# Kernel tuning notes

Measured on AMD Instinct MI355X. Metric: run time of the kernel, lower is better.

## Reference

```python
import jax, jax.numpy as jnp
import numpy as np

B, T, D = 512, 128, 256
L, CH, CS = 3, 128, 10
H = L * CH            # hidden_dim = 384
G = 4 * H + 2 * L     # gate projection width = 1542
HS = H // 6           # 64


def setup_inputs() -> dict:
    key = jax.random.key(0)
    ks = jax.random.split(key, 12)
    def lin(k, out_d, in_d):
        return jax.random.normal(k, (out_d, in_d), jnp.float32) * (1.0 / np.sqrt(in_d))
    return {
        "x": jax.random.normal(ks[0], (B, T, D), jnp.float32),
        "time": jax.random.uniform(ks[1], (B, T), jnp.float32),
        "kW": lin(ks[2], G, D + 1), "kb": jnp.zeros((G,), jnp.float32),
        "rW": lin(ks[3], G, H + 1), "rb": jnp.zeros((G,), jnp.float32),
        "sW": lin(ks[4], HS, H), "sb": jnp.zeros((HS,), jnp.float32),
        "rsW": lin(ks[5], H, HS), "rsb": jnp.zeros((H,), jnp.float32),
        "cW": lin(ks[6], H, H * CS).reshape(H, H, CS), "cb": jnp.zeros((H,), jnp.float32),
    }


def _cumax_l2r(z):
    return jnp.cumsum(jax.nn.softmax(z, axis=-1), axis=-1)


def _cumax_r2l(z):
    zf = jnp.flip(z, -1)
    return jnp.flip(jnp.cumsum(jax.nn.softmax(zf, axis=-1), axis=-1), -1)


def _forward(x, time, kW, kb, rW, rb, sW, sb, rsW, rsb, cW, cb):
    def step(carry, xt):
        c, h, buf_h, buf_d = carry
        xi, ti = xt                      # xi: (B,D), ti: (B,)
        ti = ti[:, None]
        xo = (jnp.concatenate([xi, ti], -1) @ kW.T + kb
              + jnp.concatenate([h, ti], -1) @ rW.T + rb)   # (B,G)
        fm = _cumax_l2r(xo[:, :L])[:, :, None]              # (B,L,1) master forget
        im = _cumax_r2l(xo[:, L:2 * L])[:, :, None]         # (B,L,1) master input
        g = xo[:, 2 * L:].reshape(-1, 4 * L, CH)
        fg = jax.nn.sigmoid(g[:, :L])
        ig = jax.nn.sigmoid(g[:, L:2 * L])
        og = jax.nn.sigmoid(g[:, 2 * L:3 * L])
        ci = jnp.tanh(g[:, 3 * L:])
        cl = c.reshape(-1, L, CH)
        ov = fm * im
        cn = ov * (fg * cl + ig * ci) + (fm - ov) * cl + (im - ov) * ci
        hn = og * jnp.tanh(cn)
        c_flat = cn.reshape(-1, H)
        h_flat = hn.reshape(-1, H)
        cur_dis = 1.0 - jnp.mean(fm[..., 0], axis=-1)       # (B,)
        buf_h = jnp.concatenate([buf_h[1:], h_flat[None]], 0)   # (CS,B,H)
        buf_d = jnp.concatenate([buf_d[1:], cur_dis[None]], 0)  # (CS,B)
        local_dis = jax.nn.softmax(jnp.cumsum(buf_d.T, axis=1), axis=1)  # (B,CS)
        local_h = buf_h.transpose(1, 2, 0) * local_dis[:, None, :]       # (B,H,CS)
        theme = jnp.mean(local_h, axis=-1)                               # (B,H)
        theme = jax.nn.sigmoid(jax.nn.relu(theme @ sW.T + sb) @ rsW.T + rsb)
        conv = jnp.einsum('bck,ock->bo', local_h, cW) + cb   # Conv1d over full window
        local = theme * conv
        return (c_flat, h_flat, buf_h, buf_d), (h_flat, local, cur_dis)

    z = jnp.zeros((x.shape[0], H), jnp.float32)
    carry0 = (z, z,
              jnp.zeros((CS, x.shape[0], H), jnp.float32),
              jnp.zeros((CS, x.shape[0]), jnp.float32))
    _, (origin_h, hs, dist) = jax.lax.scan(
        step, carry0, (x.transpose(1, 0, 2), time.T))
    output = hs.transpose(1, 0, 2) + origin_h.transpose(1, 0, 2)  # (B,T,H)
    last_output = output[:, -1, :]
    return last_output, output, dist  # dist: (T,B)


def reference(x, time, kW, kb, rW, rb, sW, sb, rsW, rsb, cW, cb):
    return _forward(x, time, kW, kb, rW, rb, sW, sb, rsW, rsb, cW, cb)
```

## Files before the change

kernel.cpp:

```cpp
#include <hip/hip_runtime.h>
#include <math.h>

typedef unsigned short u16;
typedef __attribute__((ext_vector_type(8))) short bf16x8;
typedef __attribute__((ext_vector_type(4))) float f32x4;

#define MFMA(a, b, c) __builtin_amdgcn_mfma_f32_16x16x32_bf16(a, b, c, 0, 0, 0)

#define Bsz 512
#define Tsz 128
#define Dsz 256
#define CSs 10
#define Hsz 384
#define Gsz 1542
#define HSz 64
#define Gp  1568
#define NGT 98
#define KTH 12
#define KTX 8
#define KTC 120

constexpr size_t O_WPK  = 0;
constexpr size_t O_XWPK = O_WPK  + 2ull*NGT*KTH*2*512;
constexpr size_t O_CPK  = O_XWPK + 2ull*NGT*KTX*2*512;
constexpr size_t O_SPK  = O_CPK  + 2ull*24*KTC*512;
constexpr size_t O_RPK  = O_SPK  + 2ull*4*KTH*2*512;
constexpr size_t O_BC   = O_RPK  + 2ull*24*2*2*512;
constexpr size_t O_WT   = O_BC + 4ull*Gp;
constexpr size_t O_HBF  = (O_WT + 4ull*Gp + 255) & ~(size_t)255;
constexpr size_t O_XPK  = O_HBF + 2ull*Bsz*Tsz*Hsz;
constexpr size_t O_XWB  = O_XPK + 2ull*Tsz*32*KTX*2*512;
constexpr size_t O_HWB  = O_XWB + 4ull*2*Bsz*Gp;
constexpr size_t O_CFB  = O_HWB + 4ull*2*Bsz*Gp;
constexpr size_t ZERO_BEG = O_CFB;
constexpr size_t ZERO_END = O_CFB + 4ull*2*Bsz*Hsz;

__device__ __forceinline__ u16 f2bf(float f) {
    unsigned u = __float_as_uint(f);
    unsigned r = (u + 0x7FFFu + ((u >> 16) & 1u)) >> 16;
    return (u16)r;
}
__device__ __forceinline__ float bf2f(u16 v) {
    return __uint_as_float(((unsigned)v) << 16);
}
__device__ __forceinline__ float sigm(float v) { return 1.f / (1.f + expf(-v)); }

__global__ __launch_bounds__(256) void zero4(float4* __restrict__ p, int n4) {
    int i = blockIdx.x * 256 + threadIdx.x;
    if (i < n4) p[i] = make_float4(0.f, 0.f, 0.f, 0.f);
}

__global__ __launch_bounds__(256) void build_w(const float* __restrict__ kW,
                                               const float* __restrict__ kb,
                                               const float* __restrict__ rW,
                                               const float* __restrict__ rb,
                                               const float* __restrict__ sW,
                                               const float* __restrict__ rsW,
                                               u16* __restrict__ wpk,
                                               u16* __restrict__ xwpk,
                                               u16* __restrict__ spk,
                                               u16* __restrict__ rpk,
                                               float* __restrict__ bc,
                                               float* __restrict__ wt) {
    const int N1 = Gp * 384, N2 = Gp * 256, N3 = 64 * 384, N4 = 384 * 64;
    int idx = blockIdx.x * 256 + threadIdx.x;
    if (idx < N1) {
        int g = idx / 384, k = idx % 384;
        float v = (g < Gsz) ? rW[g * (Hsz + 1) + k] : 0.f;
        u16 hi = f2bf(v), lo = f2bf(v - bf2f(hi));
        size_t fo = ((size_t)((g >> 4) * KTH + (k >> 5)) * 2) * 512;
        int pos = ((g & 15) | (((k >> 3) & 3) << 4)) * 8 + (k & 7);
        wpk[fo + pos] = hi; wpk[fo + 512 + pos] = lo;
    } else if (idx < N1 + N2) {
        int i = idx - N1;
        int g = i / 256, k = i % 256;
        float v = (g < Gsz) ? kW[g * (Dsz + 1) + k] : 0.f;
        u16 hi = f2bf(v), lo = f2bf(v - bf2f(hi));
        size_t fo = ((size_t)((g >> 4) * KTX + (k >> 5)) * 2) * 512;
        int pos = ((g & 15) | (((k >> 3) & 3) << 4)) * 8 + (k & 7);
        xwpk[fo + pos] = hi; xwpk[fo + 512 + pos] = lo;
    } else if (idx < N1 + N2 + N3) {
        int i = idx - N1 - N2;
        int g = i / 384, k = i % 384;
        float v = sW[g * Hsz + k];
        u16 hi = f2bf(v), lo = f2bf(v - bf2f(hi));
        size_t fo = ((size_t)((g >> 4) * KTH + (k >> 5)) * 2) * 512;
        int pos = ((g & 15) | (((k >> 3) & 3) << 4)) * 8 + (k & 7);
        spk[fo + pos] = hi; spk[fo + 512 + pos] = lo;
    } else if (idx < N1 + N2 + N3 + N4) {
        int i = idx - N1 - N2 - N3;
        int g = i / 64, k = i % 64;
        float v = rsW[g * HSz + k];
        u16 hi = f2bf(v), lo = f2bf(v - bf2f(hi));
        size_t fo = ((size_t)((g >> 4) * 2 + (k >> 5)) * 2) * 512;
        int pos = ((g & 15) | (((k >> 3) & 3) << 4)) * 8 + (k & 7);
        rpk[fo + pos] = hi; rpk[fo + 512 + pos] = lo;
    } else if (idx < N1 + N2 + N3 + N4 + Gsz) {
        int g = idx - N1 - N2 - N3 - N4;
        bc[g] = kb[g] + rb[g];
        wt[g] = kW[g * (Dsz + 1) + Dsz] + rW[g * (Hsz + 1) + Hsz];
    }
}

__global__ __launch_bounds__(256) void pack_x(const float* __restrict__ x,
                                              u16* __restrict__ xpk) {
    int idx = blockIdx.x * 256 + threadIdx.x;
    int k = idx & 255, b = (idx >> 8) & 511, t = idx >> 17;
    float v = x[((size_t)b * Tsz + t) * Dsz + k];
    u16 hi = f2bf(v), lo = f2bf(v - bf2f(hi));
    size_t fo = (((size_t)t * 32 + (b >> 4)) * KTX + (k >> 5)) * 2 * 512;
    int pos = ((b & 15) | (((k >> 3) & 3) << 4)) * 8 + (k & 7);
    xpk[fo + pos] = hi;
    xpk[fo + 512 + pos] = lo;
}

__global__ __launch_bounds__(256) void pack_cw(const float* __restrict__ cW,
                                               u16* __restrict__ cpk) {
    int idx = blockIdx.x * 256 + threadIdx.x;
    if (idx >= Hsz * Hsz * CSs) return;
    int o = idx / (Hsz * CSs), kk = idx % (Hsz * CSs);
    int ch = kk / CSs, jj = kk % CSs;
    int k2 = jj * Hsz + ch;
    size_t fo = ((size_t)(o >> 4) * KTC + (k2 >> 5)) * 512;
    int pos = ((o & 15) | (((k2 >> 3) & 3) << 4)) * 8 + (k2 & 7);
    cpk[fo + pos] = f2bf(cW[idx]);
}

__global__ __launch_bounds__(448) void fused(const float* __restrict__ tme,
                                             char* __restrict__ ws,
                                             float* __restrict__ out, int t) {
    const u16* wpk  = (const u16*)(ws + O_WPK);
    const u16* xwpk = (const u16*)(ws + O_XWPK);
    const u16* xpk  = (const u16*)(ws + O_XPK);
    const float* bc = (const float*)(ws + O_BC);
    const float* wt = (const float*)(ws + O_WT);
    float* xw = (float*)(ws + O_XWB);
    float* hw = (float*)(ws + O_HWB);
    float* cf = (float*)(ws + O_CFB);
    u16* hbf = (u16*)(ws + O_HBF);
    float* out_seq  = out + (size_t)Bsz * Hsz;
    float* out_dist = out_seq + (size_t)Bsz * Tsz * Hsz;

    int bid = blockIdx.x;
    int tid = threadIdx.x;
    int wave = tid >> 6, lane = tid & 63, l15 = lane & 15, lk = lane >> 4;
    int role = bid >> 8;
    int q = bid & 255;
    int mt = q >> 3, sbp = q & 7;

    __shared__ u16 s_h[KTH][2][512];
    __shared__ float s_fi[16][4];

    if (role == 1) {
        if (t >= Tsz) return;
        int base = sbp * 12 + (sbp < 2 ? sbp : 2);
        int cnt  = (sbp < 2) ? 13 : 12;
        const u16* Asrc = xpk + ((size_t)(t * 32 + mt) * KTX * 2) * 512;
        bf16x8 ah[KTX], al[KTX];
        #pragma unroll
        for (int kt = 0; kt < KTX; ++kt) {
            ah[kt] = *(const bf16x8*)(Asrc + (size_t)(kt * 2) * 512 + lane * 8);
            al[kt] = *(const bf16x8*)(Asrc + (size_t)(kt * 2 + 1) * 512 + lane * 8);
        }
        float* dst = xw + (size_t)(t & 1) * Bsz * Gp;
        #pragma unroll
        for (int ti = 0; ti < 2; ++ti) {
            int idx = 2 * wave + ti;
            if (idx < cnt) {
                int gt = base + idx;
                f32x4 acc = {};
                #pragma unroll
                for (int half = 0; half < 2; ++half) {
                    bf16x8 bh[4], bl[4];
                    #pragma unroll
                    for (int kk = 0; kk < 4; ++kk) {
                        int kt = half * 4 + kk;
                        size_t fb = ((size_t)(gt * KTX + kt) * 2) * 512 + lane * 8;
                        bh[kk] = *(const bf16x8*)(xwpk + fb);
                        bl[kk] = *(const bf16x8*)(xwpk + fb + 512);
                    }
                    #pragma unroll
                    for (int kk = 0; kk < 4; ++kk) {
                        int kt = half * 4 + kk;
                        acc = MFMA(ah[kt], bh[kk], acc);
                        acc = MFMA(ah[kt], bl[kk], acc);
                        acc = MFMA(al[kt], bh[kk], acc);
                    }
                }
                int col = gt * 16 + l15;
                #pragma unroll
                for (int j = 0; j < 4; ++j)
                    dst[(size_t)(mt * 16 + lk * 4 + j) * Gp + col] = acc[j];
            }
        }
        return;
    }
    if (sbp == 7) return;

    if (t == 0) {
        for (int i = tid; i < KTH * 2 * 256; i += 448) ((unsigned*)s_h)[i] = 0u;
    } else {
        const float* xw1 = xw + (size_t)((t - 1) & 1) * Bsz * Gp;
        const float* hw1 = hw + (size_t)((t - 1) & 1) * Bsz * Gp;
        const float* cfo = cf + (size_t)(t & 1) * Bsz * Hsz;
        float* cfn = cf + (size_t)((t - 1) & 1) * Bsz * Hsz;
        if (tid < 16) {
            int r = tid, b = mt * 16 + r;
            float tv = tme[b * Tsz + (t - 1)];
            const float* xr = xw1 + (size_t)b * Gp;
            const float* hr = hw1 + (size_t)b * Gp;
            float zf[6];
            #pragma unroll
            for (int g = 0; g < 6; ++g)
                zf[g] = xr[g] + hr[g] + bc[g] + tv * wt[g];
            float m = fmaxf(zf[0], fmaxf(zf[1], zf[2]));
            float e0 = expf(zf[0] - m), e1 = expf(zf[1] - m), e2 = expf(zf[2] - m);
            float inv = 1.f / (e0 + e1 + e2);
            float fm0 = e0 * inv, fm1 = fm0 + e1 * inv;
            float mw = fmaxf(zf[3], fmaxf(zf[4], zf[5]));
            float f0 = expf(zf[3] - mw), f1 = expf(zf[4] - mw), f2 = expf(zf[5] - mw);
            float invw = 1.f / (f0 + f1 + f2);
            float im2 = f2 * invw, im1 = f1 * invw + im2;
            s_fi[r][0] = fm0; s_fi[r][1] = fm1; s_fi[r][2] = im1; s_fi[r][3] = im2;
            if (sbp == 0)
                out_dist[(size_t)(t - 1) * Bsz + b] = 1.f - (fm0 + fm1 + 1.f) * (1.f / 3.f);
        }
        __syncthreads();
        if (tid < Hsz) {
            int ch = tid;
            int l = ch >> 7;
            int kt = ch >> 5;
            int g0 = 6 + ch, g1 = g0 + Hsz, g2 = g0 + 2 * Hsz, g3 = g0 + 3 * Hsz;
            float bcg0 = bc[g0], bcg1 = bc[g1], bcg2 = bc[g2], bcg3 = bc[g3];
            float wtg0 = wt[g0], wtg1 = wt[g1], wtg2 = wt[g2], wtg3 = wt[g3];
            const float* xr = xw1 + (size_t)(mt * 16) * Gp;
            const float* hr = hw1 + (size_t)(mt * 16) * Gp;
            float nx0 = xr[g0], nx1 = xr[g1], nx2 = xr[g2], nx3 = xr[g3];
            float nh0 = hr[g0], nh1 = hr[g1], nh2 = hr[g2], nh3 = hr[g3];
            for (int r = 0; r < 16; ++r) {
                float cx0 = nx0, cx1 = nx1, cx2 = nx2, cx3 = nx3;
                float hv0 = nh0, hv1 = nh1, hv2 = nh2, hv3 = nh3;
                if (r < 15) {
                    const float* xr2 = xr + (size_t)(r + 1) * Gp;
                    const float* hr2 = hr + (size_t)(r + 1) * Gp;
                    nx0 = xr2[g0]; nx1 = xr2[g1]; nx2 = xr2[g2]; nx3 = xr2[g3];
                    nh0 = hr2[g0]; nh1 = hr2[g1]; nh2 = hr2[g2]; nh3 = hr2[g3];
                }
                int b = mt * 16 + r;
                float tv = tme[b * Tsz + (t - 1)];
                float fm = (l == 0) ? s_fi[r][0] : ((l == 1) ? s_fi[r][1] : 1.f);
                float im = (l == 0) ? 1.f : ((l == 1) ? s_fi[r][2] : s_fi[r][3]);
                float fg = sigm(cx0 + hv0 + bcg0 + tv * wtg0);
                float ig = sigm(cx1 + hv1 + bcg1 + tv * wtg1);
                float og = sigm(cx2 + hv2 + bcg2 + tv * wtg2);
                float ci = tanhf(cx3 + hv3 + bcg3 + tv * wtg3);
                float cl = cfo[(size_t)b * Hsz + ch];
                float ov = fm * im;
                float cn = ov * (fg * cl + ig * ci) + (fm - ov) * cl + (im - ov) * ci;
                float hn = og * tanhf(cn);
                u16 hh = f2bf(hn);
                u16 hl = f2bf(hn - bf2f(hh));
                if (sbp == 0) {
                    cfn[(size_t)b * Hsz + ch] = cn;
                    size_t oi = ((size_t)b * Tsz + (t - 1)) * Hsz + ch;
                    out_seq[oi] = hn;
                    hbf[oi] = hh;
                }
                int pos = (r | (((ch >> 3) & 3) << 4)) * 8 + (ch & 7);
                s_h[kt][0][pos] = hh;
                s_h[kt][1][pos] = hl;
            }
        }
    }
    __syncthreads();
    if (t >= Tsz) return;

    float* dst = hw + (size_t)(t & 1) * Bsz * Gp;
    #pragma unroll
    for (int ti = 0; ti < 2; ++ti) {
        int gt = sbp * 14 + wave * 2 + ti;
        f32x4 acc = {};
        #pragma unroll
        for (int half = 0; half < 2; ++half) {
            bf16x8 bh[6], bl[6];
            #pragma unroll
            for (int kk = 0; kk < 6; ++kk) {
                int kt = half * 6 + kk;
                size_t fb = ((size_t)(gt * KTH + kt) * 2) * 512 + lane * 8;
                bh[kk] = *(const bf16x8*)(wpk + fb);
                bl[kk] = *(const bf16x8*)(wpk + fb + 512);
            }
            #pragma unroll
            for (int kk = 0; kk < 6; ++kk) {
                int kt = half * 6 + kk;
                bf16x8 ah = *(const bf16x8*)&s_h[kt][0][lane * 8];
                bf16x8 al = *(const bf16x8*)&s_h[kt][1][lane * 8];
                acc = MFMA(ah, bh[kk], acc);
                acc = MFMA(ah, bl[kk], acc);
                acc = MFMA(al, bh[kk], acc);
            }
        }
        int col = gt * 16 + l15;
        #pragma unroll
        for (int j = 0; j < 4; ++j)
            dst[(size_t)(mt * 16 + lk * 4 + j) * Gp + col] = acc[j];
    }
}

__global__ __launch_bounds__(512, 1) void post(const float* __restrict__ sb,
                                               const float* __restrict__ rsb,
                                               const float* __restrict__ cb,
                                               char* __restrict__ ws,
                                               float* __restrict__ out) {
    const u16* cpk = (const u16*)(ws + O_CPK);
    const u16* spk = (const u16*)(ws + O_SPK);
    const u16* rpk = (const u16*)(ws + O_RPK);
    const u16* hbf = (const u16*)(ws + O_HBF);

    float* out_last = out;
    float* out_seq  = out + (size_t)Bsz * Hsz;
    const float* out_dist = out_seq + (size_t)Bsz * Tsz * Hsz;

    int b = blockIdx.x, t0 = blockIdx.y * 16;
    int tid = threadIdx.x;
    int wave = tid >> 6, lane = tid & 63, l15 = lane & 15, lk = lane >> 4;

    __shared__ u16 s_apk[KTC][512];
    __shared__ u16 s_tpk[KTH * 2][512];
    __shared__ float th1s[16][68];
    __shared__ float s_ld[16][CSs];

    if (tid < 16) {
        int r = tid;
        float vals[CSs];
        float cum = 0.f;
        #pragma unroll
        for (int j = 0; j < CSs; ++j) {
            int tp = t0 + r - 9 + j;
            float d = (tp < 0) ? 0.f : out_dist[(size_t)tp * Bsz + b];
            cum += d;
            vals[j] = cum;
        }
        float mx = vals[0];
        #pragma unroll
        for (int j = 1; j < CSs; ++j) mx = fmaxf(mx, vals[j]);
        float sum = 0.f;
        #pragma unroll
        for (int j = 0; j < CSs; ++j) { vals[j] = expf(vals[j] - mx); sum += vals[j]; }
        float invs = 1.f / sum;
        #pragma unroll
        for (int j = 0; j < CSs; ++j) s_ld[r][j] = vals[j] * invs;
    }
    __syncthreads();

    for (int u = tid; u < 768; u += 512) {
        int c8 = u >> 4, r = u & 15;
        int ch0 = c8 * 8;
        int rowoff = c8 >> 2;
        int pos16 = (r | ((c8 & 3) << 4)) * 8;
        bf16x8 hv[CSs];
        #pragma unroll
        for (int j = 0; j < CSs; ++j) {
            int tp = t0 + r - 9 + j;
            bf16x8 z = {};
            hv[j] = (tp >= 0) ? *(const bf16x8*)(hbf + ((size_t)b * Tsz + tp) * Hsz + ch0) : z;
        }
        float acc[8] = {0.f, 0.f, 0.f, 0.f, 0.f, 0.f, 0.f, 0.f};
        #pragma unroll
        for (int j = 0; j < CSs; ++j) {
            float ldv = s_ld[r][j];
            bf16x8 av8;
            #pragma unroll
            for (int e = 0; e < 8; ++e) {
                float av = bf2f((u16)hv[j][e]) * ldv;
                acc[e] += av;
                av8[e] = (short)f2bf(av);
            }
            *(bf16x8*)&s_apk[j * 12 + rowoff][pos16] = av8;
        }
        bf16x8 th8, tl8;
        #pragma unroll
        for (int e = 0; e < 8; ++e) {
            float thm = acc[e] * 0.1f;
            u16 th = f2bf(thm);
            th8[e] = (short)th;
            tl8[e] = (short)f2bf(thm - bf2f(th));
        }
        int kt2 = rowoff * 2;
        *(bf16x8*)&s_tpk[kt2][pos16] = th8;
        *(bf16x8*)&s_tpk[kt2 + 1][pos16] = tl8;
    }
    __syncthreads();

    f32x4 cacc[3] = {};
    for (int k0 = 0; k0 < KTC; k0 += 8) {
        bf16x8 bv[3][8];
        #pragma unroll
        for (int kk = 0; kk < 8; ++kk)
            #pragma unroll
            for (int i = 0; i < 3; ++i)
                bv[i][kk] = *(const bf16x8*)(cpk + ((size_t)((wave * 3 + i) * KTC + k0 + kk)) * 512 + lane * 8);
        #pragma unroll
        for (int kk = 0; kk < 8; ++kk) {
            bf16x8 a = *(const bf16x8*)&s_apk[k0 + kk][lane * 8];
            #pragma unroll
            for (int i = 0; i < 3; ++i)
                cacc[i] = MFMA(a, bv[i][kk], cacc[i]);
        }
    }
    if (wave < 4) {
        f32x4 a1 = {};
        for (int kt = 0; kt < KTH; ++kt) {
            bf16x8 ah = *(const bf16x8*)&s_tpk[kt * 2][lane * 8];
            bf16x8 al = *(const bf16x8*)&s_tpk[kt * 2 + 1][lane * 8];
            size_t bb = ((size_t)(wave * KTH + kt) * 2) * 512 + lane * 8;
            bf16x8 bh = *(const bf16x8*)(spk + bb);
            bf16x8 bl = *(const bf16x8*)(spk + bb + 512);
            a1 = MFMA(ah, bh, a1);
            a1 = MFMA(ah, bl, a1);
            a1 = MFMA(al, bh, a1);
        }
        int col = wave * 16 + l15;
        #pragma unroll
        for (int j = 0; j < 4; ++j)
            th1s[lk * 4 + j][col] = fmaxf(a1[j] + sb[col], 0.f);
    }
    __syncthreads();

    bf16x8 ah2[2], al2[2];
    #pragma unroll
    for (int kt = 0; kt < 2; ++kt) {
        bf16x8 zh, zl;
        #pragma unroll
        for (int e = 0; e < 8; ++e) {
            float v = th1s[l15][kt * 32 + lk * 8 + e];
            u16 hi = f2bf(v);
            zh[e] = (short)hi;
            zl[e] = (short)f2bf(v - bf2f(hi));
        }
        ah2[kt] = zh; al2[kt] = zl;
    }
    #pragma unroll
    for (int i = 0; i < 3; ++i) {
        int ot = wave * 3 + i;
        f32x4 a2 = {};
        #pragma unroll
        for (int kt = 0; kt < 2; ++kt) {
            size_t bb = ((size_t)(ot * 2 + kt) * 2) * 512 + lane * 8;
            bf16x8 bh = *(const bf16x8*)(rpk + bb);
            bf16x8 bl = *(const bf16x8*)(rpk + bb + 512);
            a2 = MFMA(ah2[kt], bh, a2);
            a2 = MFMA(ah2[kt], bl, a2);
            a2 = MFMA(al2[kt], bh, a2);
        }
        int col = ot * 16 + l15;
        #pragma unroll
        for (int j = 0; j < 4; ++j) {
            int row = lk * 4 + j;
            int tt = t0 + row;
            size_t oi = ((size_t)b * Tsz + tt) * Hsz + col;
            float convv = cacc[i][j] + cb[col];
            float th = sigm(a2[j] + rsb[col]);
            float val = th * convv + out_seq[oi];
            out_seq[oi] = val;
            if (tt == Tsz - 1) out_last[(size_t)b * Hsz + col] = val;
        }
    }
}

extern "C" void kernel_launch(void* const* d_in, const int* in_sizes, int n_in,
                              void* d_out, int out_size, void* d_ws, size_t ws_size,
                              hipStream_t stream) {
    const float* x   = (const float*)d_in[0];
    const float* tme = (const float*)d_in[1];
    const float* kW  = (const float*)d_in[2];
    const float* kb  = (const float*)d_in[3];
    const float* rW  = (const float*)d_in[4];
    const float* rb  = (const float*)d_in[5];
    const float* sW  = (const float*)d_in[6];
    const float* sb  = (const float*)d_in[7];
    const float* rsW = (const float*)d_in[8];
    const float* rsb = (const float*)d_in[9];
    const float* cW  = (const float*)d_in[10];
    const float* cb  = (const float*)d_in[11];

    char* wsb = (char*)d_ws;
    float* outp = (float*)d_out;

    u16* wpk  = (u16*)(wsb + O_WPK);
    u16* xwpk = (u16*)(wsb + O_XWPK);
    u16* cpk  = (u16*)(wsb + O_CPK);
    u16* spk  = (u16*)(wsb + O_SPK);
    u16* rpk  = (u16*)(wsb + O_RPK);
    float* bc = (float*)(wsb + O_BC);
    float* wt = (float*)(wsb + O_WT);
    u16* xpk  = (u16*)(wsb + O_XPK);

    zero4<<<(int)((ZERO_END - ZERO_BEG) / 16 + 255) / 256, 256, 0, stream>>>(
        (float4*)(wsb + ZERO_BEG), (int)((ZERO_END - ZERO_BEG) / 16));
    {
        int nW = Gp * 384 + Gp * 256 + 64 * 384 + 384 * 64 + Gsz;
        build_w<<<(nW + 255) / 256, 256, 0, stream>>>(kW, kb, rW, rb, sW, rsW,
                                                      wpk, xwpk, spk, rpk, bc, wt);
    }
    pack_x<<<(Tsz * Bsz * Dsz) / 256, 256, 0, stream>>>(x, xpk);
    pack_cw<<<(Hsz * Hsz * CSs + 255) / 256, 256, 0, stream>>>(cW, cpk);

    for (int t = 0; t <= Tsz; ++t)
        fused<<<512, 448, 0, stream>>>(tme, wsb, outp, t);
    post<<<dim3(Bsz, Tsz / 16), 512, 0, stream>>>(sb, rsb, cb, wsb, outp);
}
```

Before: 3.682 ms.

## Precompute input projection for all timesteps in one batched kernel before recurrence

The x@kW input projection for every timestep is computed up front in a single large kernel into a workspace buffer, instead of being computed by half of the blocks inside each per-step fused launch. The recurrent launches then use half the grid and read the precomputed slice for step t-1. This moves off-critical-path work out of the sequential loop, at the cost of about 400MB of extra workspace and extra memory traffic. It falls back to the old path if the workspace is too small.

```diff
diff --git a/kernel.cpp b/kernel.cpp
--- a/kernel.cpp
+++ b/kernel.cpp
@@ -15,6 +15,7 @@
 #define Gsz 1542
 #define HSz 64
 #define Gp  1568
+#define BG  ((size_t)Bsz * Gp)
 #define NGT 98
 #define KTH 12
 #define KTX 8
@@ -30,10 +31,12 @@
 constexpr size_t O_HBF  = (O_WT + 4ull*Gp + 255) & ~(size_t)255;
 constexpr size_t O_XPK  = O_HBF + 2ull*Bsz*Tsz*Hsz;
 constexpr size_t O_XWB  = O_XPK + 2ull*Tsz*32*KTX*2*512;
-constexpr size_t O_HWB  = O_XWB + 4ull*2*Bsz*Gp;
-constexpr size_t O_CFB  = O_HWB + 4ull*2*Bsz*Gp;
+constexpr size_t O_HWB  = O_XWB + 4ull*2*BG;
+constexpr size_t O_CFB  = O_HWB + 4ull*2*BG;
 constexpr size_t ZERO_BEG = O_CFB;
 constexpr size_t ZERO_END = O_CFB + 4ull*2*Bsz*Hsz;
+constexpr size_t O_XWALL = (ZERO_END + 255) & ~(size_t)255;
+constexpr size_t NEED_ALL = O_XWALL + 4ull*Tsz*BG;
 
 __device__ __forceinline__ u16 f2bf(float f) {
     unsigned u = __float_as_uint(f);
@@ -126,9 +129,67 @@
     cpk[fo + pos] = f2bf(cW[idx]);
 }
 
+__device__ __forceinline__ void xw_slab(const u16* __restrict__ xwpk,
+                                        const u16* __restrict__ xpk,
+                                        float* __restrict__ dst,
+                                        int t, int mt, int sbp,
+                                        int wave, int lane, int l15, int lk) {
+    int base = sbp * 12 + (sbp < 2 ? sbp : 2);
+    int cnt  = (sbp < 2) ? 13 : 12;
+    const u16* Asrc = xpk + ((size_t)(t * 32 + mt) * KTX * 2) * 512;
+    bf16x8 ah[KTX], al[KTX];
+    #pragma unroll
+    for (int kt = 0; kt < KTX; ++kt) {
+        ah[kt] = *(const bf16x8*)(Asrc + (size_t)(kt * 2) * 512 + lane * 8);
+        al[kt] = *(const bf16x8*)(Asrc + (size_t)(kt * 2 + 1) * 512 + lane * 8);
+    }
+    #pragma unroll
+    for (int ti = 0; ti < 2; ++ti) {
+        int idx = 2 * wave + ti;
+        if (idx < cnt) {
+            int gt = base + idx;
+            f32x4 acc = {};
+            #pragma unroll
+            for (int half = 0; half < 2; ++half) {
+                bf16x8 bh[4], bl[4];
+                #pragma unroll
+                for (int kk = 0; kk < 4; ++kk) {
+                    int kt = half * 4 + kk;
+                    size_t fb = ((size_t)(gt * KTX + kt) * 2) * 512 + lane * 8;
+                    bh[kk] = *(const bf16x8*)(xwpk + fb);
+                    bl[kk] = *(const bf16x8*)(xwpk + fb + 512);
+                }
+                #pragma unroll
+                for (int kk = 0; kk < 4; ++kk) {
+                    int kt = half * 4 + kk;
+                    acc = MFMA(ah[kt], bh[kk], acc);
+                    acc = MFMA(ah[kt], bl[kk], acc);
+                    acc = MFMA(al[kt], bh[kk], acc);
+                }
+            }
+            int col = gt * 16 + l15;
+            #pragma unroll
+            for (int j = 0; j < 4; ++j)
+                dst[(size_t)(mt * 16 + lk * 4 + j) * Gp + col] = acc[j];
+        }
+    }
+}
+
+__global__ __launch_bounds__(448) void xwall_k(char* __restrict__ ws) {
+    const u16* xwpk = (const u16*)(ws + O_XWPK);
+    const u16* xpk  = (const u16*)(ws + O_XPK);
+    float* xwall = (float*)(ws + O_XWALL);
+    int q = blockIdx.x, t = blockIdx.y;
+    int mt = q >> 3, sbp = q & 7;
+    int wave = threadIdx.x >> 6, lane = threadIdx.x & 63;
+    xw_slab(xwpk, xpk, xwall + (size_t)t * BG, t, mt, sbp,
+            wave, lane, lane & 15, lane >> 4);
+}
+
 __global__ __launch_bounds__(448) void fused(const float* __restrict__ tme,
                                              char* __restrict__ ws,
-                                             float* __restrict__ out, int t) {
+                                             float* __restrict__ out, int t,
+                                             int use_all) {
     const u16* wpk  = (const u16*)(ws + O_WPK);
     const u16* xwpk = (const u16*)(ws + O_XWPK);
     const u16* xpk  = (const u16*)(ws + O_XPK);
@@ -153,46 +214,8 @@
 
     if (role == 1) {
         if (t >= Tsz) return;
-        int base = sbp * 12 + (sbp < 2 ? sbp : 2);
-        int cnt  = (sbp < 2) ? 13 : 12;
-        const u16* Asrc = xpk + ((size_t)(t * 32 + mt) * KTX * 2) * 512;
-        bf16x8 ah[KTX], al[KTX];
-        #pragma unroll
-        for (int kt = 0; kt < KTX; ++kt) {
-            ah[kt] = *(const bf16x8*)(Asrc + (size_t)(kt * 2) * 512 + lane * 8);
-            al[kt] = *(const bf16x8*)(Asrc + (size_t)(kt * 2 + 1) * 512 + lane * 8);
-        }
-        float* dst = xw + (size_t)(t & 1) * Bsz * Gp;
-        #pragma unroll
-        for (int ti = 0; ti < 2; ++ti) {
-            int idx = 2 * wave + ti;
-            if (idx < cnt) {
-                int gt = base + idx;
-                f32x4 acc = {};
-                #pragma unroll
-                for (int half = 0; half < 2; ++half) {
-                    bf16x8 bh[4], bl[4];
-                    #pragma unroll
-                    for (int kk = 0; kk < 4; ++kk) {
-                        int kt = half * 4 + kk;
-                        size_t fb = ((size_t)(gt * KTX + kt) * 2) * 512 + lane * 8;
-                        bh[kk] = *(const bf16x8*)(xwpk + fb);
-                        bl[kk] = *(const bf16x8*)(xwpk + fb + 512);
-                    }
-                    #pragma unroll
-                    for (int kk = 0; kk < 4; ++kk) {
-                        int kt = half * 4 + kk;
-                        acc = MFMA(ah[kt], bh[kk], acc);
-                        acc = MFMA(ah[kt], bl[kk], acc);
-                        acc = MFMA(al[kt], bh[kk], acc);
-                    }
-                }
-                int col = gt * 16 + l15;
-                #pragma unroll
-                for (int j = 0; j < 4; ++j)
-                    dst[(size_t)(mt * 16 + lk * 4 + j) * Gp + col] = acc[j];
-            }
-        }
+        float* dst = xw + (size_t)(t & 1) * BG;
+        xw_slab(xwpk, xpk, dst, t, mt, sbp, wave, lane, l15, lk);
         return;
     }
     if (sbp == 7) return;
@@ -200,8 +223,9 @@
     if (t == 0) {
         for (int i = tid; i < KTH * 2 * 256; i += 448) ((unsigned*)s_h)[i] = 0u;
     } else {
-        const float* xw1 = xw + (size_t)((t - 1) & 1) * Bsz * Gp;
-        const float* hw1 = hw + (size_t)((t - 1) & 1) * Bsz * Gp;
+        const float* xw1 = use_all ? (const float*)(ws + O_XWALL) + (size_t)(t - 1) * BG
+                                   : xw + (size_t)((t - 1) & 1) * BG;
+        const float* hw1 = hw + (size_t)((t - 1) & 1) * BG;
         const float* cfo = cf + (size_t)(t & 1) * Bsz * Hsz;
         float* cfn = cf + (size_t)((t - 1) & 1) * Bsz * Hsz;
         if (tid < 16) {
@@ -275,7 +299,7 @@
     __syncthreads();
     if (t >= Tsz) return;
 
-    float* dst = hw + (size_t)(t & 1) * Bsz * Gp;
+    float* dst = hw + (size_t)(t & 1) * BG;
     #pragma unroll
     for (int ti = 0; ti < 2; ++ti) {
         int gt = sbp * 14 + wave * 2 + ti;
@@ -496,6 +520,8 @@
     float* wt = (float*)(wsb + O_WT);
     u16* xpk  = (u16*)(wsb + O_XPK);
 
+    int use_all = (ws_size >= NEED_ALL) ? 1 : 0;
+
     zero4<<<(int)((ZERO_END - ZERO_BEG) / 16 + 255) / 256, 256, 0, stream>>>(
         (float4*)(wsb + ZERO_BEG), (int)((ZERO_END - ZERO_BEG) / 16));
     {
@@ -506,7 +532,11 @@
     pack_x<<<(Tsz * Bsz * Dsz) / 256, 256, 0, stream>>>(x, xpk);
     pack_cw<<<(Hsz * Hsz * CSs + 255) / 256, 256, 0, stream>>>(cW, cpk);
 
+    if (use_all)
+        xwall_k<<<dim3(256, Tsz), 448, 0, stream>>>(wsb);
+
+    int grid = use_all ? 256 : 512;
     for (int t = 0; t <= Tsz; ++t)
-        fused<<<512, 448, 0, stream>>>(tme, wsb, outp, t);
+        fused<<<grid, 448, 0, stream>>>(tme, wsb, outp, t, use_all);
     post<<<dim3(Bsz, Tsz / 16), 512, 0, stream>>>(sb, rsb, cb, wsb, outp);
 }
```

Result: no change. 3.660 ms (-0.6%).

## Merge x-projection and recurrent roles into one 1024-thread block per tile

Applied to the files above, without the earlier changes.

The per-step kernel used to launch 512 blocks of 448 threads, half computing the input projection and half the recurrent update plus hidden projection. It now launches 256 blocks of 1024 threads, each doing both jobs. Each wave handles one gate tile instead of two, and the elementwise cell update is split across twice as many threads, eight rows each instead of sixteen. The aim is to shorten the serial per-step critical path through more wave-level parallelism, at the cost of bigger blocks with one block per CU and more register pressure.

```diff
diff --git a/kernel.cpp b/kernel.cpp
--- a/kernel.cpp
+++ b/kernel.cpp
@@ -15,6 +15,7 @@
 #define Gsz 1542
 #define HSz 64
 #define Gp  1568
+#define BG  ((size_t)Bsz * Gp)
 #define NGT 98
 #define KTH 12
 #define KTX 8
@@ -30,8 +31,8 @@
 constexpr size_t O_HBF  = (O_WT + 4ull*Gp + 255) & ~(size_t)255;
 constexpr size_t O_XPK  = O_HBF + 2ull*Bsz*Tsz*Hsz;
 constexpr size_t O_XWB  = O_XPK + 2ull*Tsz*32*KTX*2*512;
-constexpr size_t O_HWB  = O_XWB + 4ull*2*Bsz*Gp;
-constexpr size_t O_CFB  = O_HWB + 4ull*2*Bsz*Gp;
+constexpr size_t O_HWB  = O_XWB + 4ull*2*BG;
+constexpr size_t O_CFB  = O_HWB + 4ull*2*BG;
 constexpr size_t ZERO_BEG = O_CFB;
 constexpr size_t ZERO_END = O_CFB + 4ull*2*Bsz*Hsz;
 
@@ -126,9 +127,9 @@
     cpk[fo + pos] = f2bf(cW[idx]);
 }
 
-__global__ __launch_bounds__(448) void fused(const float* __restrict__ tme,
-                                             char* __restrict__ ws,
-                                             float* __restrict__ out, int t) {
+__global__ __launch_bounds__(1024, 1) void fused(const float* __restrict__ tme,
+                                                 char* __restrict__ ws,
+                                                 float* __restrict__ out, int t) {
     const u16* wpk  = (const u16*)(ws + O_WPK);
     const u16* xwpk = (const u16*)(ws + O_XWPK);
     const u16* xpk  = (const u16*)(ws + O_XPK);
@@ -144,166 +145,159 @@
     int bid = blockIdx.x;
     int tid = threadIdx.x;
     int wave = tid >> 6, lane = tid & 63, l15 = lane & 15, lk = lane >> 4;
-    int role = bid >> 8;
-    int q = bid & 255;
-    int mt = q >> 3, sbp = q & 7;
+    int mt = bid >> 3, sbp = bid & 7;
 
     __shared__ u16 s_h[KTH][2][512];
     __shared__ float s_fi[16][4];
 
-    if (role == 1) {
-        if (t >= Tsz) return;
+    if (sbp < 7) {
+        if (t == 0) {
+            for (int i = tid; i < KTH * 2 * 256; i += 1024) ((unsigned*)s_h)[i] = 0u;
+        } else {
+            const float* xw1 = xw + (size_t)((t - 1) & 1) * BG;
+            const float* hw1 = hw + (size_t)((t - 1) & 1) * BG;
+            const float* cfo = cf + (size_t)(t & 1) * Bsz * Hsz;
+            float* cfn = cf + (size_t)((t - 1) & 1) * Bsz * Hsz;
+            if (tid < 16) {
+                int r = tid, b = mt * 16 + r;
+                float tv = tme[b * Tsz + (t - 1)];
+                const float* xr = xw1 + (size_t)b * Gp;
+                const float* hr = hw1 + (size_t)b * Gp;
+                float zf[6];
+                #pragma unroll
+                for (int g = 0; g < 6; ++g)
+                    zf[g] = xr[g] + hr[g] + bc[g] + tv * wt[g];
+                float m = fmaxf(zf[0], fmaxf(zf[1], zf[2]));
+                float e0 = expf(zf[0] - m), e1 = expf(zf[1] - m), e2 = expf(zf[2] - m);
+                float inv = 1.f / (e0 + e1 + e2);
+                float fm0 = e0 * inv, fm1 = fm0 + e1 * inv;
+                float mw = fmaxf(zf[3], fmaxf(zf[4], zf[5]));
+                float f0 = expf(zf[3] - mw), f1 = expf(zf[4] - mw), f2 = expf(zf[5] - mw);
+                float invw = 1.f / (f0 + f1 + f2);
+                float im2 = f2 * invw, im1 = f1 * invw + im2;
+                s_fi[r][0] = fm0; s_fi[r][1] = fm1; s_fi[r][2] = im1; s_fi[r][3] = im2;
+                if (sbp == 0)
+                    out_dist[(size_t)(t - 1) * Bsz + b] = 1.f - (fm0 + fm1 + 1.f) * (1.f / 3.f);
+            }
+            __syncthreads();
+            if (tid < 768) {
+                int ch = tid >> 1;
+                int rh = tid & 1;
+                int l = ch >> 7;
+                int kt = ch >> 5;
+                int g0 = 6 + ch, g1 = g0 + Hsz, g2 = g0 + 2 * Hsz, g3 = g0 + 3 * Hsz;
+                float bcg0 = bc[g0], bcg1 = bc[g1], bcg2 = bc[g2], bcg3 = bc[g3];
+                float wtg0 = wt[g0], wtg1 = wt[g1], wtg2 = wt[g2], wtg3 = wt[g3];
+                const float* xr = xw1 + (size_t)(mt * 16 + rh * 8) * Gp;
+                const float* hr = hw1 + (size_t)(mt * 16 + rh * 8) * Gp;
+                float nx0 = xr[g0], nx1 = xr[g1], nx2 = xr[g2], nx3 = xr[g3];
+                float nh0 = hr[g0], nh1 = hr[g1], nh2 = hr[g2], nh3 = hr[g3];
+                for (int r2 = 0; r2 < 8; ++r2) {
+                    float cx0 = nx0, cx1 = nx1, cx2 = nx2, cx3 = nx3;
+                    float hv0 = nh0, hv1 = nh1, hv2 = nh2, hv3 = nh3;
+                    if (r2 < 7) {
+                        const float* xr2 = xr + (size_t)(r2 + 1) * Gp;
+                        const float* hr2 = hr + (size_t)(r2 + 1) * Gp;
+                        nx0 = xr2[g0]; nx1 = xr2[g1]; nx2 = xr2[g2]; nx3 = xr2[g3];
+                        nh0 = hr2[g0]; nh1 = hr2[g1]; nh2 = hr2[g2]; nh3 = hr2[g3];
+                    }
+                    int r = rh * 8 + r2;
+                    int b = mt * 16 + r;
+                    float tv = tme[b * Tsz + (t - 1)];
+                    float fm = (l == 0) ? s_fi[r][0] : ((l == 1) ? s_fi[r][1] : 1.f);
+                    float im = (l == 0) ? 1.f : ((l == 1) ? s_fi[r][2] : s_fi[r][3]);
+                    float fg = sigm(cx0 + hv0 + bcg0 + tv * wtg0);
+                    float ig = sigm(cx1 + hv1 + bcg1 + tv * wtg1);
+                    float og = sigm(cx2 + hv2 + bcg2 + tv * wtg2);
+                    float ci = tanhf(cx3 + hv3 + bcg3 + tv * wtg3);
+                    float cl = cfo[(size_t)b * Hsz + ch];
+                    float ov = fm * im;
+                    float cn = ov * (fg * cl + ig * ci) + (fm - ov) * cl + (im - ov) * ci;
+                    float hn = og * tanhf(cn);
+                    u16 hh = f2bf(hn);
+                    u16 hl = f2bf(hn - bf2f(hh));
+                    if (sbp == 0) {
+                        cfn[(size_t)b * Hsz + ch] = cn;
+                        size_t oi = ((size_t)b * Tsz + (t - 1)) * Hsz + ch;
+                        out_seq[oi] = hn;
+                        hbf[oi] = hh;
+                    }
+                    int pos = (r | (((ch >> 3) & 3) << 4)) * 8 + (ch & 7);
+                    s_h[kt][0][pos] = hh;
+                    s_h[kt][1][pos] = hl;
+                }
+            }
+        }
+        __syncthreads();
+
+        if (t < Tsz && wave < 14) {
+            int gt = sbp * 14 + wave;
+            float* dst = hw + (size_t)(t & 1) * BG;
+            f32x4 acc = {};
+            #pragma unroll
+            for (int half = 0; half < 2; ++half) {
+                bf16x8 bh[6], bl[6];
+                #pragma unroll
+                for (int kk = 0; kk < 6; ++kk) {
+                    int kt = half * 6 + kk;
+                    size_t fb = ((size_t)(gt * KTH + kt) * 2) * 512 + lane * 8;
+                    bh[kk] = *(const bf16x8*)(wpk + fb);
+                    bl[kk] = *(const bf16x8*)(wpk + fb + 512);
+                }
+                #pragma unroll
+                for (int kk = 0; kk < 6; ++kk) {
+                    int kt = half * 6 + kk;
+                    bf16x8 ah = *(const bf16x8*)&s_h[kt][0][lane * 8];
+                    bf16x8 al = *(const bf16x8*)&s_h[kt][1][lane * 8];
+                    acc = MFMA(ah, bh[kk], acc);
+                    acc = MFMA(ah, bl[kk], acc);
+                    acc = MFMA(al, bh[kk], acc);
+                }
+            }
+            int col = gt * 16 + l15;
+            #pragma unroll
+            for (int j = 0; j < 4; ++j)
+                dst[(size_t)(mt * 16 + lk * 4 + j) * Gp + col] = acc[j];
+        }
+    }
+
+    if (t < Tsz) {
         int base = sbp * 12 + (sbp < 2 ? sbp : 2);
         int cnt  = (sbp < 2) ? 13 : 12;
-        const u16* Asrc = xpk + ((size_t)(t * 32 + mt) * KTX * 2) * 512;
-        bf16x8 ah[KTX], al[KTX];
-        #pragma unroll
-        for (int kt = 0; kt < KTX; ++kt) {
-            ah[kt] = *(const bf16x8*)(Asrc + (size_t)(kt * 2) * 512 + lane * 8);
-            al[kt] = *(const bf16x8*)(Asrc + (size_t)(kt * 2 + 1) * 512 + lane * 8);
-        }
-        float* dst = xw + (size_t)(t & 1) * Bsz * Gp;
-        #pragma unroll
-        for (int ti = 0; ti < 2; ++ti) {
-            int idx = 2 * wave + ti;
-            if (idx < cnt) {
-                int gt = base + idx;
-                f32x4 acc = {};
+        if (wave < cnt) {
+            int gt = base + wave;
+            const u16* Asrc = xpk + ((size_t)(t * 32 + mt) * KTX * 2) * 512;
+            bf16x8 ah[KTX], al[KTX];
+            #pragma unroll
+            for (int kt = 0; kt < KTX; ++kt) {
+                ah[kt] = *(const bf16x8*)(Asrc + (size_t)(kt * 2) * 512 + lane * 8);
+                al[kt] = *(const bf16x8*)(Asrc + (size_t)(kt * 2 + 1) * 512 + lane * 8);
+            }
+            float* dst = xw + (size_t)(t & 1) * BG;
+            f32x4 acc = {};
+            #pragma unroll
+            for (int half = 0; half < 2; ++half) {
+                bf16x8 bh[4], bl[4];
                 #pragma unroll
-                for (int half = 0; half < 2; ++half) {
-                    bf16x8 bh[4], bl[4];
-                    #pragma unroll
-                    for (int kk = 0; kk < 4; ++kk) {
-                        int kt = half * 4 + kk;
-                        size_t fb = ((size_t)(gt * KTX + kt) * 2) * 512 + lane * 8;
-                        bh[kk] = *(const bf16x8*)(xwpk + fb);
-                        bl[kk] = *(const bf16x8*)(xwpk + fb + 512);
-                    }
-                    #pragma unroll
-                    for (int kk = 0; kk < 4; ++kk) {
-                        int kt = half * 4 + kk;
-                        acc = MFMA(ah[kt], bh[kk], acc);
-                        acc = MFMA(ah[kt], bl[kk], acc);
-                        acc = MFMA(al[kt], bh[kk], acc);
-                    }
+                for (int kk = 0; kk < 4; ++kk) {
+                    int kt = half * 4 + kk;
+                    size_t fb = ((size_t)(gt * KTX + kt) * 2) * 512 + lane * 8;
+                    bh[kk] = *(const bf16x8*)(xwpk + fb);
+                    bl[kk] = *(const bf16x8*)(xwpk + fb + 512);
                 }
-                int col = gt * 16 + l15;
                 #pragma unroll
-                for (int j = 0; j < 4; ++j)
-                    dst[(size_t)(mt * 16 + lk * 4 + j) * Gp + col] = acc[j];
+                for (int kk = 0; kk < 4; ++kk) {
+                    int kt = half * 4 + kk;
+                    acc = MFMA(ah[kt], bh[kk], acc);
+                    acc = MFMA(ah[kt], bl[kk], acc);
+                    acc = MFMA(al[kt], bh[kk], acc);
+                }
             }
-        }
-        return;
-    }
-    if (sbp == 7) return;
-
-    if (t == 0) {
-        for (int i = tid; i < KTH * 2 * 256; i += 448) ((unsigned*)s_h)[i] = 0u;
-    } else {
-        const float* xw1 = xw + (size_t)((t - 1) & 1) * Bsz * Gp;
-        const float* hw1 = hw + (size_t)((t - 1) & 1) * Bsz * Gp;
-        const float* cfo = cf + (size_t)(t & 1) * Bsz * Hsz;
-        float* cfn = cf + (size_t)((t - 1) & 1) * Bsz * Hsz;
-        if (tid < 16) {
-            int r = tid, b = mt * 16 + r;
-            float tv = tme[b * Tsz + (t - 1)];
-            const float* xr = xw1 + (size_t)b * Gp;
-            const float* hr = hw1 + (size_t)b * Gp;
-            float zf[6];
-            #pragma unroll
-            for (int g = 0; g < 6; ++g)
-                zf[g] = xr[g] + hr[g] + bc[g] + tv * wt[g];
-            float m = fmaxf(zf[0], fmaxf(zf[1], zf[2]));
-            float e0 = expf(zf[0] - m), e1 = expf(zf[1] - m), e2 = expf(zf[2] - m);
-            float inv = 1.f / (e0 + e1 + e2);
-            float fm0 = e0 * inv, fm1 = fm0 + e1 * inv;
-            float mw = fmaxf(zf[3], fmaxf(zf[4], zf[5]));
-            float f0 = expf(zf[3] - mw), f1 = expf(zf[4] - mw), f2 = expf(zf[5] - mw);
-            float invw = 1.f / (f0 + f1 + f2);
-            float im2 = f2 * invw, im1 = f1 * invw + im2;
-            s_fi[r][0] = fm0; s_fi[r][1] = fm1; s_fi[r][2] = im1; s_fi[r][3] = im2;
-            if (sbp == 0)
-                out_dist[(size_t)(t - 1) * Bsz + b] = 1.f - (fm0 + fm1 + 1.f) * (1.f / 3.f);
-        }
-        __syncthreads();
-        if (tid < Hsz) {
-            int ch = tid;
-            int l = ch >> 7;
-            int kt = ch >> 5;
-            int g0 = 6 + ch, g1 = g0 + Hsz, g2 = g0 + 2 * Hsz, g3 = g0 + 3 * Hsz;
-            float bcg0 = bc[g0], bcg1 = bc[g1], bcg2 = bc[g2], bcg3 = bc[g3];
-            float wtg0 = wt[g0], wtg1 = wt[g1], wtg2 = wt[g2], wtg3 = wt[g3];
-            const float* xr = xw1 + (size_t)(mt * 16) * Gp;
-            const float* hr = hw1 + (size_t)(mt * 16) * Gp;
-            float nx0 = xr[g0], nx1 = xr[g1], nx2 = xr[g2], nx3 = xr[g3];
-            float nh0 = hr[g0], nh1 = hr[g1], nh2 = hr[g2], nh3 = hr[g3];
-            for (int r = 0; r < 16; ++r) {
-                float cx0 = nx0, cx1 = nx1, cx2 = nx2, cx3 = nx3;
-                float hv0 = nh0, hv1 = nh1, hv2 = nh2, hv3 = nh3;
-                if (r < 15) {
-                    const float* xr2 = xr + (size_t)(r + 1) * Gp;
-                    const float* hr2 = hr + (size_t)(r + 1) * Gp;
-                    nx0 = xr2[g0]; nx1 = xr2[g1]; nx2 = xr2[g2]; nx3 = xr2[g3];
-                    nh0 = hr2[g0]; nh1 = hr2[g1]; nh2 = hr2[g2]; nh3 = hr2[g3];
-                }
-                int b = mt * 16 + r;
-                float tv = tme[b * Tsz + (t - 1)];
-                float fm = (l == 0) ? s_fi[r][0] : ((l == 1) ? s_fi[r][1] : 1.f);
-                float im = (l == 0) ? 1.f : ((l == 1) ? s_fi[r][2] : s_fi[r][3]);
-                float fg = sigm(cx0 + hv0 + bcg0 + tv * wtg0);
-                float ig = sigm(cx1 + hv1 + bcg1 + tv * wtg1);
-                float og = sigm(cx2 + hv2 + bcg2 + tv * wtg2);
-                float ci = tanhf(cx3 + hv3 + bcg3 + tv * wtg3);
-                float cl = cfo[(size_t)b * Hsz + ch];
-                float ov = fm * im;
-                float cn = ov * (fg * cl + ig * ci) + (fm - ov) * cl + (im - ov) * ci;
-                float hn = og * tanhf(cn);
-                u16 hh = f2bf(hn);
-                u16 hl = f2bf(hn - bf2f(hh));
-                if (sbp == 0) {
-                    cfn[(size_t)b * Hsz + ch] = cn;
-                    size_t oi = ((size_t)b * Tsz + (t - 1)) * Hsz + ch;
-                    out_seq[oi] = hn;
-                    hbf[oi] = hh;
-                }
-                int pos = (r | (((ch >> 3) & 3) << 4)) * 8 + (ch & 7);
-                s_h[kt][0][pos] = hh;
-                s_h[kt][1][pos] = hl;
-            }
-        }
-    }
-    __syncthreads();
-    if (t >= Tsz) return;
-
-    float* dst = hw + (size_t)(t & 1) * Bsz * Gp;
-    #pragma unroll
-    for (int ti = 0; ti < 2; ++ti) {
-        int gt = sbp * 14 + wave * 2 + ti;
-        f32x4 acc = {};
-        #pragma unroll
-        for (int half = 0; half < 2; ++half) {
-            bf16x8 bh[6], bl[6];
-            #pragma unroll
-            for (int kk = 0; kk < 6; ++kk) {
-                int kt = half * 6 + kk;
-                size_t fb = ((size_t)(gt * KTH + kt) * 2) * 512 + lane * 8;
-                bh[kk] = *(const bf16x8*)(wpk + fb);
-                bl[kk] = *(const bf16x8*)(wpk + fb + 512);
-            }
-            #pragma unroll
-            for (int kk = 0; kk < 6; ++kk) {
-                int kt = half * 6 + kk;
-                bf16x8 ah = *(const bf16x8*)&s_h[kt][0][lane * 8];
-                bf16x8 al = *(const bf16x8*)&s_h[kt][1][lane * 8];
-                acc = MFMA(ah, bh[kk], acc);
-                acc = MFMA(ah, bl[kk], acc);
-                acc = MFMA(al, bh[kk], acc);
-            }
-        }
-        int col = gt * 16 + l15;
-        #pragma unroll
-        for (int j = 0; j < 4; ++j)
-            dst[(size_t)(mt * 16 + lk * 4 + j) * Gp + col] = acc[j];
+            int col = gt * 16 + l15;
+            #pragma unroll
+            for (int j = 0; j < 4; ++j)
+                dst[(size_t)(mt * 16 + lk * 4 + j) * Gp + col] = acc[j];
+        }
     }
 }
 
@@ -507,6 +501,6 @@
     pack_cw<<<(Hsz * Hsz * CSs + 255) / 256, 256, 0, stream>>>(cW, cpk);
 
     for (int t = 0; t <= Tsz; ++t)
-        fused<<<512, 448, 0, stream>>>(tme, wsb, outp, t);
+        fused<<<256, 1024, 0, stream>>>(tme, wsb, outp, t);
     post<<<dim3(Bsz, Tsz / 16), 512, 0, stream>>>(sb, rsb, cb, wsb, outp);
 }
```

Measured after the change: 3.571 ms. 1.03x faster.
